# Performance work log

Hardware: AMD Instinct MI355X
Metric: run time of the kernel (lower is better)

The kernel has to match this reference:

```python
import jax, jax.numpy as jnp
import numpy as np

DIM = 1024
HEADS = 16
DIM_HEAD = 64
INNER = HEADS * DIM_HEAD
SCALE = 8.0  # default scale in plain_cosine_sim_attention
EPS = 1e-5


def setup_inputs() -> dict:
    key = jax.random.key(0)
    ks = jax.random.split(key, 5)
    b, n = 2, 2048
    x = jax.random.normal(ks[0], (b, n, DIM), dtype=jnp.float32)
    ln_w = jnp.ones((DIM,), dtype=jnp.float32)
    ln_b = jnp.zeros((DIM,), dtype=jnp.float32)
    W_qkv = jax.random.normal(ks[1], (DIM, 3 * INNER), dtype=jnp.float32) * (DIM ** -0.5)
    W_out = jax.random.normal(ks[2], (INNER, DIM), dtype=jnp.float32) * (INNER ** -0.5)
    return {"x": x, "ln_w": ln_w, "ln_b": ln_b, "W_qkv": W_qkv, "W_out": W_out}


def _l2norm(t):
    return t / jnp.clip(jnp.linalg.norm(t, axis=-1, keepdims=True), 1e-12)


def reference(x, ln_w, ln_b, W_qkv, W_out):
    b, n, _ = x.shape
    # LayerNorm
    mu = jnp.mean(x, axis=-1, keepdims=True)
    var = jnp.var(x, axis=-1, keepdims=True)
    xn = (x - mu) * jax.lax.rsqrt(var + EPS) * ln_w + ln_b
    # QKV projection (no bias)
    qkv = xn @ W_qkv  # [b, n, 3*inner]
    q, k, v = jnp.split(qkv, 3, axis=-1)
    # [b, n, h*d] -> [b, h, n, d]
    def to_heads(t):
        return t.reshape(b, n, HEADS, DIM_HEAD).transpose(0, 2, 1, 3)
    q, k, v = to_heads(q), to_heads(k), to_heads(v)
    # cosine-sim attention: l2-normalize q, k then scaled dot product
    q = _l2norm(q)
    k = _l2norm(k)
    sim = jnp.einsum('bhid,bhjd->bhij', q, k) * SCALE
    # causal mask
    causal = jnp.tril(jnp.ones((n, n), dtype=bool))
    sim = jnp.where(causal, sim, jnp.finfo(sim.dtype).min)
    attn = jax.nn.softmax(sim, axis=-1)
    o = jnp.einsum('bhij,bhjd->bhid', attn, v)
    # [b, h, n, d] -> [b, n, h*d]
    o = o.transpose(0, 2, 1, 3).reshape(b, n, INNER)
    return o @ W_out
```

## Files before the change

### kernel.cpp

```cpp
#include <hip/hip_runtime.h>
#include <hip/hip_bf16.h>

typedef __attribute__((ext_vector_type(8))) short short8;
typedef __attribute__((ext_vector_type(4))) float floatx4;

__device__ __forceinline__ ushort f2bf(float f) {
    union { __hip_bfloat16 h; ushort u; } cv;
    cv.h = __float2bfloat16(f);
    return cv.u;
}
__device__ __forceinline__ float bf2f(ushort u) {
    union { ushort u; __hip_bfloat16 h; } cv;
    cv.u = u;
    return __bfloat162float(cv.h);
}

typedef __attribute__((address_space(1))) void* gas1_t;
typedef __attribute__((address_space(3))) void* las3_t;
__device__ __forceinline__ void cp16(const ushort* g, ushort* l) {
    __builtin_amdgcn_global_load_lds((gas1_t)(unsigned long long)g,
                                     (las3_t)(unsigned long long)l, 16, 0, 0);
}

__global__ __launch_bounds__(256) void transpose_cast(const float* __restrict__ in,
                                                      ushort* __restrict__ out,
                                                      int R, int C) {
    __shared__ float tile[32][33];
    int c0 = blockIdx.x * 32, r0 = blockIdx.y * 32;
    int tx = threadIdx.x, ty = threadIdx.y;
    for (int j = 0; j < 32; j += 8)
        tile[ty + j][tx] = in[(size_t)(r0 + ty + j) * C + c0 + tx];
    __syncthreads();
    for (int j = 0; j < 32; j += 8)
        out[(size_t)(c0 + ty + j) * R + r0 + tx] = f2bf(tile[tx][ty + j]);
}

__global__ __launch_bounds__(256) void ln_kernel(const float* __restrict__ x,
                                                 const float* __restrict__ lw,
                                                 const float* __restrict__ lb,
                                                 ushort* __restrict__ xn) {
    int row = blockIdx.x;
    int tid = threadIdx.x;
    const float4* xr = (const float4*)(x + (size_t)row * 1024);
    float4 v = xr[tid];
    float s = v.x + v.y + v.z + v.w;
    float sq = v.x * v.x + v.y * v.y + v.z * v.z + v.w * v.w;
    for (int off = 32; off; off >>= 1) {
        s += __shfl_xor(s, off);
        sq += __shfl_xor(sq, off);
    }
    __shared__ float ls[4], lq[4];
    int wave = tid >> 6, lane = tid & 63;
    if (lane == 0) { ls[wave] = s; lq[wave] = sq; }
    __syncthreads();
    s = ls[0] + ls[1] + ls[2] + ls[3];
    sq = lq[0] + lq[1] + lq[2] + lq[3];
    float mu = s * (1.0f / 1024.0f);
    float var = sq * (1.0f / 1024.0f) - mu * mu;
    float rs = rsqrtf(var + 1e-5f);
    const float4* wr = (const float4*)lw;
    const float4* br = (const float4*)lb;
    float4 wv = wr[tid], bv = br[tid];
    ushort4 o;
    o.x = f2bf((v.x - mu) * rs * wv.x + bv.x);
    o.y = f2bf((v.y - mu) * rs * wv.y + bv.y);
    o.z = f2bf((v.z - mu) * rs * wv.z + bv.z);
    o.w = f2bf((v.w - mu) * rs * wv.w + bv.w);
    *(ushort4*)&xn[(size_t)row * 1024 + tid * 4] = o;
}

template <typename OutT>
__global__ __launch_bounds__(256) void gemm_bt(const ushort* __restrict__ A,
                                               const ushort* __restrict__ Bt,
                                               OutT* __restrict__ C,
                                               int M, int N, int K) {
    __shared__ ushort As[128 * 32];
    __shared__ ushort Bs[128 * 32];
    const int tid = threadIdx.x;
    const int wave = tid >> 6, lane = tid & 63;
    const int quad = lane >> 4, l15 = lane & 15;
    const int wm = (wave >> 1) * 64, wn = (wave & 1) * 64;
    const int bm = blockIdx.y * 128, bn = blockIdx.x * 128;

    const int s0 = tid, s1 = tid + 256;
    const int row0 = s0 >> 2, src0 = (s0 & 3) ^ (row0 & 3);
    const int row1 = s1 >> 2, src1 = (s1 & 3) ^ (row1 & 3);

    floatx4 acc[4][4];
    floatx4 z4 = {0.f, 0.f, 0.f, 0.f};
    for (int mi = 0; mi < 4; mi++)
        for (int ni = 0; ni < 4; ni++) acc[mi][ni] = z4;

    const ushort* Ap0 = A + (size_t)(bm + row0) * K + src0 * 8;
    const ushort* Ap1 = A + (size_t)(bm + row1) * K + src1 * 8;
    const ushort* Bp0 = Bt + (size_t)(bn + row0) * K + src0 * 8;
    const ushort* Bp1 = Bt + (size_t)(bn + row1) * K + src1 * 8;

    ushort* lA0 = As + wave * 512;
    ushort* lA1 = As + 2048 + wave * 512;
    ushort* lB0 = Bs + wave * 512;
    ushort* lB1 = Bs + 2048 + wave * 512;

    for (int k0 = 0; k0 < K; k0 += 32) {
        __syncthreads();
        cp16(Ap0 + k0, lA0);
        cp16(Ap1 + k0, lA1);
        cp16(Bp0 + k0, lB0);
        cp16(Bp1 + k0, lB1);
        __syncthreads();
        short8 af[4], bfr[4];
        for (int mi = 0; mi < 4; mi++) {
            int ra = wm + mi * 16 + l15;
            af[mi] = *(short8*)&As[ra * 32 + ((quad ^ (ra & 3)) << 3)];
        }
        for (int ni = 0; ni < 4; ni++) {
            int rb = wn + ni * 16 + l15;
            bfr[ni] = *(short8*)&Bs[rb * 32 + ((quad ^ (rb & 3)) << 3)];
        }
        for (int mi = 0; mi < 4; mi++)
            for (int ni = 0; ni < 4; ni++)
                acc[mi][ni] = __builtin_amdgcn_mfma_f32_16x16x32_bf16(
                    af[mi], bfr[ni], acc[mi][ni], 0, 0, 0);
    }
    for (int mi = 0; mi < 4; mi++) {
        for (int ni = 0; ni < 4; ni++) {
            for (int r = 0; r < 4; r++) {
                int row = bm + wm + mi * 16 + quad * 4 + r;
                int col = bn + wn + ni * 16 + l15;
                float val = acc[mi][ni][r];
                if constexpr (sizeof(OutT) == 2)
                    ((ushort*)C)[(size_t)row * N + col] = f2bf(val);
                else
                    ((float*)C)[(size_t)row * N + col] = val;
            }
        }
    }
}

__global__ __launch_bounds__(256) void norm_reshape(const ushort* __restrict__ qkv,
                                                    ushort* __restrict__ Q,
                                                    ushort* __restrict__ K,
                                                    ushort* __restrict__ Vt) {
    int nb = blockIdx.x;
    int h = blockIdx.y;
    int b = blockIdx.z;
    int bh = b * 16 + h;
    int tid = threadIdx.x, wave = tid >> 6, lane = tid & 63;
    __shared__ ushort vt[64][65];

    for (int i = 0; i < 16; i++) {
        int idx = tid + i * 256;
        int n_loc = idx >> 6, d = idx & 63;
        size_t g = ((size_t)(b * 2048 + nb * 64 + n_loc)) * 3072 + 2048 + h * 64 + d;
        vt[d][n_loc] = qkv[g];
    }
    __syncthreads();
    for (int i = 0; i < 16; i++) {
        int idx = tid + i * 256;
        int d = idx >> 6, n_loc = idx & 63;
        Vt[((size_t)bh * 64 + d) * 2048 + nb * 64 + n_loc] = vt[d][n_loc];
    }

    for (int j = 0; j < 16; j++) {
        int n_loc = wave * 16 + j;
        size_t grow = (size_t)(b * 2048 + nb * 64 + n_loc) * 3072;
        size_t orow = ((size_t)bh * 2048 + nb * 64 + n_loc) * 64;

        float qv = bf2f(qkv[grow + h * 64 + lane]);
        float ss = qv * qv;
        for (int off = 32; off; off >>= 1) ss += __shfl_xor(ss, off);
        float inv = 1.0f / fmaxf(sqrtf(ss), 1e-12f);
        Q[orow + lane] = f2bf(qv * inv);

        float kv = bf2f(qkv[grow + 1024 + h * 64 + lane]);
        ss = kv * kv;
        for (int off = 32; off; off >>= 1) ss += __shfl_xor(ss, off);
        inv = 1.0f / fmaxf(sqrtf(ss), 1e-12f);
        K[orow + lane] = f2bf(kv * inv);
    }
}

#define BH_STRIDE (2048 * 64)
#define LOG2E8 11.541560327111707f

__global__ __launch_bounds__(512) void flash_attn(const ushort* __restrict__ Q,
                                                  const ushort* __restrict__ K,
                                                  const ushort* __restrict__ Vt,
                                                  ushort* __restrict__ O) {
    const int pairi = blockIdx.x;
    const int h = blockIdx.y;
    const int b = blockIdx.z;
    const int bh = b * 16 + h;
    const int tid = threadIdx.x;
    const int wave = tid >> 6, lane = tid & 63;
    const int quad = lane >> 4, l15 = lane & 15;

    __shared__ ushort Qs[128 * 72];
    __shared__ ushort Ks[64 * 72];
    __shared__ ushort Vs[64 * 72];
    __shared__ ushort Ps[8][16 * 72];

    const ushort* Kg = K + (size_t)bh * BH_STRIDE;
    const ushort* Vg = Vt + (size_t)bh * BH_STRIDE;

    const int srow = tid >> 3, sseg = tid & 7;
    const ushort* kp = Kg + (size_t)srow * 64 + sseg * 8;
    const ushort* vp = Vg + (size_t)srow * 2048 + sseg * 8;
    ushort* ksl = &Ks[srow * 72 + sseg * 8];
    ushort* vsl = &Vs[srow * 72 + sseg * 8];

    for (int pass = 0; pass < 2; pass++) {
        const int st = pass ? (15 - pairi) : pairi;
        const int q0 = st * 128;
        const int ktmax = 2 * st + 1;
        const ushort* Qg = Q + (size_t)bh * BH_STRIDE + (size_t)q0 * 64;

        __syncthreads();
        for (int i = 0; i < 2; i++) {
            int s = tid + i * 512;
            int row = s >> 3, seg = s & 7;
            *(short8*)&Qs[row * 72 + seg * 8] = *(const short8*)&Qg[(size_t)row * 64 + seg * 8];
        }
        short8 kreg = *(const short8*)kp;
        short8 vreg = *(const short8*)vp;
        __syncthreads();
        short8 qf0 = *(short8*)&Qs[(wave * 16 + l15) * 72 + quad * 8];
        short8 qf1 = *(short8*)&Qs[(wave * 16 + l15) * 72 + 32 + quad * 8];

        float rs_acc[4] = {0.f, 0.f, 0.f, 0.f};
        floatx4 o_acc[4];
        floatx4 z4 = {0.f, 0.f, 0.f, 0.f};
        for (int ni = 0; ni < 4; ni++) o_acc[ni] = z4;
        const int wrow_min = q0 + wave * 16;
        const int wrow_max = wrow_min + 15;

        for (int kt = 0; kt <= ktmax; kt++) {
            const int kv0 = kt * 64;
            __syncthreads();
            *(short8*)ksl = kreg;
            *(short8*)vsl = vreg;
            __syncthreads();
            if (kt < ktmax) {
                kreg = *(const short8*)&kp[(size_t)(kt + 1) * 4096];
                vreg = *(const short8*)&vp[(size_t)(kt + 1) * 64];
            }
            if (kv0 > wrow_max) continue;

            floatx4 s_acc[4];
            for (int ni = 0; ni < 4; ni++) s_acc[ni] = z4;
            for (int ni = 0; ni < 4; ni++) {
                short8 bf0 = *(short8*)&Ks[(ni * 16 + l15) * 72 + quad * 8];
                short8 bf1 = *(short8*)&Ks[(ni * 16 + l15) * 72 + 32 + quad * 8];
                s_acc[ni] = __builtin_amdgcn_mfma_f32_16x16x32_bf16(qf0, bf0, s_acc[ni], 0, 0, 0);
                s_acc[ni] = __builtin_amdgcn_mfma_f32_16x16x32_bf16(qf1, bf1, s_acc[ni], 0, 0, 0);
            }

            if (kv0 + 63 > wrow_min) {
                for (int ni = 0; ni < 4; ni++) {
                    int col = kv0 + ni * 16 + l15;
                    for (int r = 0; r < 4; r++) {
                        int row = wrow_min + quad * 4 + r;
                        float e = exp2f(fmaf(s_acc[ni][r], LOG2E8, -LOG2E8));
                        e = (col > row) ? 0.f : e;
                        rs_acc[r] += e;
                        Ps[wave][(quad * 4 + r) * 72 + ni * 16 + l15] = f2bf(e);
                    }
                }
            } else {
                for (int ni = 0; ni < 4; ni++) {
                    for (int r = 0; r < 4; r++) {
                        float e = exp2f(fmaf(s_acc[ni][r], LOG2E8, -LOG2E8));
                        rs_acc[r] += e;
                        Ps[wave][(quad * 4 + r) * 72 + ni * 16 + l15] = f2bf(e);
                    }
                }
            }

            short8 pa0 = *(short8*)&Ps[wave][l15 * 72 + quad * 8];
            short8 pa1 = *(short8*)&Ps[wave][l15 * 72 + 32 + quad * 8];
            for (int ni = 0; ni < 4; ni++) {
                short8 v0 = *(short8*)&Vs[(ni * 16 + l15) * 72 + quad * 8];
                short8 v1 = *(short8*)&Vs[(ni * 16 + l15) * 72 + 32 + quad * 8];
                o_acc[ni] = __builtin_amdgcn_mfma_f32_16x16x32_bf16(pa0, v0, o_acc[ni], 0, 0, 0);
                o_acc[ni] = __builtin_amdgcn_mfma_f32_16x16x32_bf16(pa1, v1, o_acc[ni], 0, 0, 0);
            }
        }

        for (int r = 0; r < 4; r++) {
            float rs = rs_acc[r];
            for (int off = 1; off < 16; off <<= 1) rs += __shfl_xor(rs, off);
            float inv = 1.0f / rs;
            int grow = q0 + wave * 16 + quad * 4 + r;
            size_t rowbase = ((size_t)b * 2048 + grow) * 1024 + h * 64;
            for (int ni = 0; ni < 4; ni++)
                O[rowbase + ni * 16 + l15] = f2bf(o_acc[ni][r] * inv);
        }
    }
}

extern "C" void kernel_launch(void* const* d_in, const int* in_sizes, int n_in,
                              void* d_out, int out_size, void* d_ws, size_t ws_size,
                              hipStream_t stream) {
    const float* x = (const float*)d_in[0];
    const float* ln_w = (const float*)d_in[1];
    const float* ln_b = (const float*)d_in[2];
    const float* W_qkv = (const float*)d_in[3];
    const float* W_out = (const float*)d_in[4];

    char* w = (char*)d_ws;
    ushort* xn    = (ushort*)(w);
    ushort* WqkvT = (ushort*)(w + (8ull << 20));
    ushort* WoutT = (ushort*)(w + (14ull << 20));
    ushort* qkv   = (ushort*)(w + (16ull << 20));
    ushort* Qn    = (ushort*)(w + (40ull << 20));
    ushort* Kn    = (ushort*)(w + (48ull << 20));
    ushort* Vt    = (ushort*)(w + (56ull << 20));
    ushort* obuf  = (ushort*)(w + (64ull << 20));

    transpose_cast<<<dim3(96, 32), dim3(32, 8), 0, stream>>>(W_qkv, WqkvT, 1024, 3072);
    transpose_cast<<<dim3(32, 32), dim3(32, 8), 0, stream>>>(W_out, WoutT, 1024, 1024);
    ln_kernel<<<4096, 256, 0, stream>>>(x, ln_w, ln_b, xn);
    gemm_bt<ushort><<<dim3(24, 32), 256, 0, stream>>>(xn, WqkvT, qkv, 4096, 3072, 1024);
    norm_reshape<<<dim3(32, 16, 2), 256, 0, stream>>>(qkv, Qn, Kn, Vt);
    flash_attn<<<dim3(8, 16, 2), 512, 0, stream>>>(Qn, Kn, Vt, obuf);
    gemm_bt<float><<<dim3(8, 32), 256, 0, stream>>>(obuf, WoutT, (float*)d_out, 4096, 1024, 1024);
}
```

Baseline: 212.5 us.

## Double-buffer GEMM and attention loads, fold L2 norms into score scaling

The GEMM now double-buffers its LDS tiles so the next K-slice's direct-to-LDS loads overlap the current MFMAs, dropping one barrier per iteration. The attention kernel reads raw Q/K straight from the qkv buffer and applies the per-row inverse norms (computed by a slimmer prep kernel) as scale factors inside the exponent. It also uses 64-row query tiles with 256 threads, XOR-swizzled double-buffered K/V tiles loaded via global_load_lds, raw exp2, and truncating bf16 conversion of probabilities. Vectorized V transposes cut prep cost. The risks are small precision changes from applying the norms after the bf16 matmul and from truncating P, plus a changed occupancy and grid shape.

```diff
diff --git a/kernel.cpp b/kernel.cpp
--- a/kernel.cpp
+++ b/kernel.cpp
@@ -13,6 +13,11 @@
     union { ushort u; __hip_bfloat16 h; } cv;
     cv.u = u;
     return __bfloat162float(cv.h);
+}
+__device__ __forceinline__ ushort f2bf_rtz(float f) {
+    union { float f; unsigned u; } cv;
+    cv.f = f;
+    return (ushort)(cv.u >> 16);
 }
 
 typedef __attribute__((address_space(1))) void* gas1_t;
@@ -74,8 +79,8 @@
                                                const ushort* __restrict__ Bt,
                                                OutT* __restrict__ C,
                                                int M, int N, int K) {
-    __shared__ ushort As[128 * 32];
-    __shared__ ushort Bs[128 * 32];
+    __shared__ ushort As[2][128 * 32];
+    __shared__ ushort Bs[2][128 * 32];
     const int tid = threadIdx.x;
     const int wave = tid >> 6, lane = tid & 63;
     const int quad = lane >> 4, l15 = lane & 15;
@@ -96,26 +101,32 @@
     const ushort* Bp0 = Bt + (size_t)(bn + row0) * K + src0 * 8;
     const ushort* Bp1 = Bt + (size_t)(bn + row1) * K + src1 * 8;
 
-    ushort* lA0 = As + wave * 512;
-    ushort* lA1 = As + 2048 + wave * 512;
-    ushort* lB0 = Bs + wave * 512;
-    ushort* lB1 = Bs + 2048 + wave * 512;
-
-    for (int k0 = 0; k0 < K; k0 += 32) {
+    const int T = K >> 5;
+    cp16(Ap0, &As[0][wave * 512]);
+    cp16(Ap1, &As[0][2048 + wave * 512]);
+    cp16(Bp0, &Bs[0][wave * 512]);
+    cp16(Bp1, &Bs[0][2048 + wave * 512]);
+
+    for (int t = 0; t < T; t++) {
         __syncthreads();
-        cp16(Ap0 + k0, lA0);
-        cp16(Ap1 + k0, lA1);
-        cp16(Bp0 + k0, lB0);
-        cp16(Bp1 + k0, lB1);
-        __syncthreads();
+        if (t + 1 < T) {
+            const int nb = (t + 1) & 1;
+            const int k0n = (t + 1) << 5;
+            cp16(Ap0 + k0n, &As[nb][wave * 512]);
+            cp16(Ap1 + k0n, &As[nb][2048 + wave * 512]);
+            cp16(Bp0 + k0n, &Bs[nb][wave * 512]);
+            cp16(Bp1 + k0n, &Bs[nb][2048 + wave * 512]);
+        }
+        const ushort* Ab = As[t & 1];
+        const ushort* Bb = Bs[t & 1];
         short8 af[4], bfr[4];
         for (int mi = 0; mi < 4; mi++) {
             int ra = wm + mi * 16 + l15;
-            af[mi] = *(short8*)&As[ra * 32 + ((quad ^ (ra & 3)) << 3)];
+            af[mi] = *(const short8*)&Ab[ra * 32 + ((quad ^ (ra & 3)) << 3)];
         }
         for (int ni = 0; ni < 4; ni++) {
             int rb = wn + ni * 16 + l15;
-            bfr[ni] = *(short8*)&Bs[rb * 32 + ((quad ^ (rb & 3)) << 3)];
+            bfr[ni] = *(const short8*)&Bb[rb * 32 + ((quad ^ (rb & 3)) << 3)];
         }
         for (int mi = 0; mi < 4; mi++)
             for (int ni = 0; ni < 4; ni++)
@@ -137,54 +148,52 @@
     }
 }
 
-__global__ __launch_bounds__(256) void norm_reshape(const ushort* __restrict__ qkv,
-                                                    ushort* __restrict__ Q,
-                                                    ushort* __restrict__ K,
-                                                    ushort* __restrict__ Vt) {
-    int nb = blockIdx.x;
-    int h = blockIdx.y;
-    int b = blockIdx.z;
-    int bh = b * 16 + h;
-    int tid = threadIdx.x, wave = tid >> 6, lane = tid & 63;
-    __shared__ ushort vt[64][65];
-
-    for (int i = 0; i < 16; i++) {
-        int idx = tid + i * 256;
-        int n_loc = idx >> 6, d = idx & 63;
-        size_t g = ((size_t)(b * 2048 + nb * 64 + n_loc)) * 3072 + 2048 + h * 64 + d;
-        vt[d][n_loc] = qkv[g];
+__global__ __launch_bounds__(256) void prep(const ushort* __restrict__ qkv,
+                                            ushort* __restrict__ Vt,
+                                            float* __restrict__ qn,
+                                            float* __restrict__ kn) {
+    const int nb = blockIdx.x;
+    const int h = blockIdx.y;
+    const int b = blockIdx.z;
+    const int bh = b * 16 + h;
+    const int tid = threadIdx.x, wave = tid >> 6, lane = tid & 63;
+    __shared__ ushort vt[64][72];
+
+    union S8 { short8 v; ushort u[8]; };
+    for (int i = 0; i < 2; i++) {
+        int c = tid + i * 256;
+        int nl = c >> 3, sg = c & 7;
+        S8 vv;
+        vv.v = *(const short8*)&qkv[(size_t)(b * 2048 + nb * 64 + nl) * 3072 + 2048 + h * 64 + sg * 8];
+        for (int j = 0; j < 8; j++) vt[sg * 8 + j][nl] = vv.u[j];
     }
     __syncthreads();
-    for (int i = 0; i < 16; i++) {
-        int idx = tid + i * 256;
-        int d = idx >> 6, n_loc = idx & 63;
-        Vt[((size_t)bh * 64 + d) * 2048 + nb * 64 + n_loc] = vt[d][n_loc];
+    for (int i = 0; i < 2; i++) {
+        int c = tid + i * 256;
+        int d = c >> 3, sg = c & 7;
+        *(short8*)&Vt[((size_t)bh * 64 + d) * 2048 + nb * 64 + sg * 8] =
+            *(const short8*)&vt[d][sg * 8];
     }
 
     for (int j = 0; j < 16; j++) {
-        int n_loc = wave * 16 + j;
-        size_t grow = (size_t)(b * 2048 + nb * 64 + n_loc) * 3072;
-        size_t orow = ((size_t)bh * 2048 + nb * 64 + n_loc) * 64;
-
-        float qv = bf2f(qkv[grow + h * 64 + lane]);
+        int nl = wave * 16 + j;
+        size_t rowb = (size_t)(b * 2048 + nb * 64 + nl) * 3072 + h * 64;
+        float qv = bf2f(qkv[rowb + lane]);
         float ss = qv * qv;
         for (int off = 32; off; off >>= 1) ss += __shfl_xor(ss, off);
-        float inv = 1.0f / fmaxf(sqrtf(ss), 1e-12f);
-        Q[orow + lane] = f2bf(qv * inv);
-
-        float kv = bf2f(qkv[grow + 1024 + h * 64 + lane]);
+        if (lane == 0) qn[(size_t)bh * 2048 + nb * 64 + nl] = 1.0f / fmaxf(sqrtf(ss), 1e-12f);
+        float kv = bf2f(qkv[rowb + 1024 + lane]);
         ss = kv * kv;
         for (int off = 32; off; off >>= 1) ss += __shfl_xor(ss, off);
-        inv = 1.0f / fmaxf(sqrtf(ss), 1e-12f);
-        K[orow + lane] = f2bf(kv * inv);
-    }
-}
-
-#define BH_STRIDE (2048 * 64)
+        if (lane == 0) kn[(size_t)bh * 2048 + nb * 64 + nl] = 1.0f / fmaxf(sqrtf(ss), 1e-12f);
+    }
+}
+
 #define LOG2E8 11.541560327111707f
 
-__global__ __launch_bounds__(512) void flash_attn(const ushort* __restrict__ Q,
-                                                  const ushort* __restrict__ K,
+__global__ __launch_bounds__(256) void flash_attn(const ushort* __restrict__ qkv,
+                                                  const float* __restrict__ qn,
+                                                  const float* __restrict__ kn,
                                                   const ushort* __restrict__ Vt,
                                                   ushort* __restrict__ O) {
     const int pairi = blockIdx.x;
@@ -195,92 +204,86 @@
     const int wave = tid >> 6, lane = tid & 63;
     const int quad = lane >> 4, l15 = lane & 15;
 
-    __shared__ ushort Qs[128 * 72];
-    __shared__ ushort Ks[64 * 72];
-    __shared__ ushort Vs[64 * 72];
-    __shared__ ushort Ps[8][16 * 72];
-
-    const ushort* Kg = K + (size_t)bh * BH_STRIDE;
-    const ushort* Vg = Vt + (size_t)bh * BH_STRIDE;
-
-    const int srow = tid >> 3, sseg = tid & 7;
-    const ushort* kp = Kg + (size_t)srow * 64 + sseg * 8;
-    const ushort* vp = Vg + (size_t)srow * 2048 + sseg * 8;
-    ushort* ksl = &Ks[srow * 72 + sseg * 8];
-    ushort* vsl = &Vs[srow * 72 + sseg * 8];
+    __shared__ ushort Ks[2][64 * 64];
+    __shared__ ushort Vs[2][64 * 64];
+    __shared__ ushort Ps[4][16 * 72];
+
+    const int ch0 = tid, ch1 = tid + 256;
+    const int r0 = ch0 >> 3, sg0 = (ch0 & 7) ^ (r0 & 7);
+    const int r1 = ch1 >> 3, sg1 = (ch1 & 7) ^ (r1 & 7);
+
+    const ushort* Kp0 = qkv + (size_t)(b * 2048 + r0) * 3072 + 1024 + h * 64 + sg0 * 8;
+    const ushort* Kp1 = qkv + (size_t)(b * 2048 + r1) * 3072 + 1024 + h * 64 + sg1 * 8;
+    const ushort* Vp0 = Vt + ((size_t)bh * 64 + r0) * 2048 + sg0 * 8;
+    const ushort* Vp1 = Vt + ((size_t)bh * 64 + r1) * 2048 + sg1 * 8;
+
+    const float* knb = kn + (size_t)bh * 2048;
+    floatx4 z4 = {0.f, 0.f, 0.f, 0.f};
 
     for (int pass = 0; pass < 2; pass++) {
-        const int st = pass ? (15 - pairi) : pairi;
-        const int q0 = st * 128;
-        const int ktmax = 2 * st + 1;
-        const ushort* Qg = Q + (size_t)bh * BH_STRIDE + (size_t)q0 * 64;
-
-        __syncthreads();
-        for (int i = 0; i < 2; i++) {
-            int s = tid + i * 512;
-            int row = s >> 3, seg = s & 7;
-            *(short8*)&Qs[row * 72 + seg * 8] = *(const short8*)&Qg[(size_t)row * 64 + seg * 8];
-        }
-        short8 kreg = *(const short8*)kp;
-        short8 vreg = *(const short8*)vp;
-        __syncthreads();
-        short8 qf0 = *(short8*)&Qs[(wave * 16 + l15) * 72 + quad * 8];
-        short8 qf1 = *(short8*)&Qs[(wave * 16 + l15) * 72 + 32 + quad * 8];
+        const int st = pass ? (31 - pairi) : pairi;
+        const int q0 = st * 64;
+
+        const ushort* Qp = qkv + (size_t)(b * 2048 + q0 + wave * 16 + l15) * 3072 + h * 64;
+        short8 qf0 = *(const short8*)(Qp + quad * 8);
+        short8 qf1 = *(const short8*)(Qp + 32 + quad * 8);
+        float a_r[4];
+        for (int r = 0; r < 4; r++)
+            a_r[r] = LOG2E8 * qn[(size_t)bh * 2048 + q0 + wave * 16 + quad * 4 + r];
 
         float rs_acc[4] = {0.f, 0.f, 0.f, 0.f};
         floatx4 o_acc[4];
-        floatx4 z4 = {0.f, 0.f, 0.f, 0.f};
         for (int ni = 0; ni < 4; ni++) o_acc[ni] = z4;
-        const int wrow_min = q0 + wave * 16;
-        const int wrow_max = wrow_min + 15;
-
-        for (int kt = 0; kt <= ktmax; kt++) {
+
+        __syncthreads();
+        cp16(Kp0, &Ks[0][wave * 512]);
+        cp16(Kp1, &Ks[0][2048 + wave * 512]);
+        cp16(Vp0, &Vs[0][wave * 512]);
+        cp16(Vp1, &Vs[0][2048 + wave * 512]);
+
+        for (int kt = 0; kt <= st; kt++) {
             const int kv0 = kt * 64;
             __syncthreads();
-            *(short8*)ksl = kreg;
-            *(short8*)vsl = vreg;
-            __syncthreads();
-            if (kt < ktmax) {
-                kreg = *(const short8*)&kp[(size_t)(kt + 1) * 4096];
-                vreg = *(const short8*)&vp[(size_t)(kt + 1) * 64];
-            }
-            if (kv0 > wrow_max) continue;
+            if (kt < st) {
+                const int nb2 = (kt + 1) & 1;
+                const size_t ko = (size_t)(kv0 + 64) * 3072;
+                cp16(Kp0 + ko, &Ks[nb2][wave * 512]);
+                cp16(Kp1 + ko, &Ks[nb2][2048 + wave * 512]);
+                cp16(Vp0 + kv0 + 64, &Vs[nb2][wave * 512]);
+                cp16(Vp1 + kv0 + 64, &Vs[nb2][2048 + wave * 512]);
+            }
+            const ushort* Kb = Ks[kt & 1];
+            const ushort* Vb = Vs[kt & 1];
 
             floatx4 s_acc[4];
             for (int ni = 0; ni < 4; ni++) s_acc[ni] = z4;
             for (int ni = 0; ni < 4; ni++) {
-                short8 bf0 = *(short8*)&Ks[(ni * 16 + l15) * 72 + quad * 8];
-                short8 bf1 = *(short8*)&Ks[(ni * 16 + l15) * 72 + 32 + quad * 8];
-                s_acc[ni] = __builtin_amdgcn_mfma_f32_16x16x32_bf16(qf0, bf0, s_acc[ni], 0, 0, 0);
-                s_acc[ni] = __builtin_amdgcn_mfma_f32_16x16x32_bf16(qf1, bf1, s_acc[ni], 0, 0, 0);
-            }
-
-            if (kv0 + 63 > wrow_min) {
-                for (int ni = 0; ni < 4; ni++) {
-                    int col = kv0 + ni * 16 + l15;
-                    for (int r = 0; r < 4; r++) {
-                        int row = wrow_min + quad * 4 + r;
-                        float e = exp2f(fmaf(s_acc[ni][r], LOG2E8, -LOG2E8));
-                        e = (col > row) ? 0.f : e;
-                        rs_acc[r] += e;
-                        Ps[wave][(quad * 4 + r) * 72 + ni * 16 + l15] = f2bf(e);
-                    }
+                int rb = ni * 16 + l15;
+                short8 kf0 = *(const short8*)&Kb[rb * 64 + ((quad ^ (rb & 7)) << 3)];
+                short8 kf1 = *(const short8*)&Kb[rb * 64 + (((quad + 4) ^ (rb & 7)) << 3)];
+                s_acc[ni] = __builtin_amdgcn_mfma_f32_16x16x32_bf16(qf0, kf0, s_acc[ni], 0, 0, 0);
+                s_acc[ni] = __builtin_amdgcn_mfma_f32_16x16x32_bf16(qf1, kf1, s_acc[ni], 0, 0, 0);
+            }
+
+            const bool diag = (kt == st);
+            for (int ni = 0; ni < 4; ni++) {
+                const int col_loc = ni * 16 + l15;
+                const float knv = knb[kv0 + col_loc];
+                for (int r = 0; r < 4; r++) {
+                    float e = __builtin_amdgcn_exp2f(
+                        fmaf(s_acc[ni][r] * knv, a_r[r], -LOG2E8));
+                    if (diag && col_loc > wave * 16 + quad * 4 + r) e = 0.f;
+                    rs_acc[r] += e;
+                    Ps[wave][(quad * 4 + r) * 72 + col_loc] = f2bf_rtz(e);
                 }
-            } else {
-                for (int ni = 0; ni < 4; ni++) {
-                    for (int r = 0; r < 4; r++) {
-                        float e = exp2f(fmaf(s_acc[ni][r], LOG2E8, -LOG2E8));
-                        rs_acc[r] += e;
-                        Ps[wave][(quad * 4 + r) * 72 + ni * 16 + l15] = f2bf(e);
-                    }
-                }
-            }
-
-            short8 pa0 = *(short8*)&Ps[wave][l15 * 72 + quad * 8];
-            short8 pa1 = *(short8*)&Ps[wave][l15 * 72 + 32 + quad * 8];
+            }
+
+            short8 pa0 = *(const short8*)&Ps[wave][l15 * 72 + quad * 8];
+            short8 pa1 = *(const short8*)&Ps[wave][l15 * 72 + 32 + quad * 8];
             for (int ni = 0; ni < 4; ni++) {
-                short8 v0 = *(short8*)&Vs[(ni * 16 + l15) * 72 + quad * 8];
-                short8 v1 = *(short8*)&Vs[(ni * 16 + l15) * 72 + 32 + quad * 8];
+                int rv = ni * 16 + l15;
+                short8 v0 = *(const short8*)&Vb[rv * 64 + ((quad ^ (rv & 7)) << 3)];
+                short8 v1 = *(const short8*)&Vb[rv * 64 + (((quad + 4) ^ (rv & 7)) << 3)];
                 o_acc[ni] = __builtin_amdgcn_mfma_f32_16x16x32_bf16(pa0, v0, o_acc[ni], 0, 0, 0);
                 o_acc[ni] = __builtin_amdgcn_mfma_f32_16x16x32_bf16(pa1, v1, o_acc[ni], 0, 0, 0);
             }
@@ -312,16 +315,16 @@
     ushort* WqkvT = (ushort*)(w + (8ull << 20));
     ushort* WoutT = (ushort*)(w + (14ull << 20));
     ushort* qkv   = (ushort*)(w + (16ull << 20));
-    ushort* Qn    = (ushort*)(w + (40ull << 20));
-    ushort* Kn    = (ushort*)(w + (48ull << 20));
-    ushort* Vt    = (ushort*)(w + (56ull << 20));
-    ushort* obuf  = (ushort*)(w + (64ull << 20));
+    ushort* Vt    = (ushort*)(w + (40ull << 20));
+    float*  qn    = (float*)(w + (48ull << 20));
+    float*  kn    = (float*)(w + (49ull << 20));
+    ushort* obuf  = (ushort*)(w + (50ull << 20));
 
     transpose_cast<<<dim3(96, 32), dim3(32, 8), 0, stream>>>(W_qkv, WqkvT, 1024, 3072);
     transpose_cast<<<dim3(32, 32), dim3(32, 8), 0, stream>>>(W_out, WoutT, 1024, 1024);
     ln_kernel<<<4096, 256, 0, stream>>>(x, ln_w, ln_b, xn);
     gemm_bt<ushort><<<dim3(24, 32), 256, 0, stream>>>(xn, WqkvT, qkv, 4096, 3072, 1024);
-    norm_reshape<<<dim3(32, 16, 2), 256, 0, stream>>>(qkv, Qn, Kn, Vt);
-    flash_attn<<<dim3(8, 16, 2), 512, 0, stream>>>(Qn, Kn, Vt, obuf);
+    prep<<<dim3(32, 16, 2), 256, 0, stream>>>(qkv, Vt, qn, kn);
+    flash_attn<<<dim3(16, 16, 2), 256, 0, stream>>>(qkv, qn, kn, Vt, obuf);
     gemm_bt<float><<<dim3(8, 32), 256, 0, stream>>>(obuf, WoutT, (float*)d_out, 4096, 1024, 1024);
 }
```

New measurement: 207.8 us. 2.2% less time.
